# Performance work log

Hardware: AMD Instinct MI355X
Metric: run time of the kernel (lower is better)

Reference implementation:

```python
import jax, jax.numpy as jnp
import numpy as np


def setup_inputs() -> dict:
    key = jax.random.key(0)
    ks = jax.random.split(key, 6)
    B, d, S = 256, 512, 196  # batch, hidden dim, spatial locations (14x14)
    return {
        "memory_state": jax.random.normal(ks[0], (B, d), dtype=jnp.float32),
        "ctrl_state": jax.random.normal(ks[1], (B, d), dtype=jnp.float32),
        "kb_proj": jax.random.normal(ks[2], (B, d, S), dtype=jnp.float32),
        "W_concat": jax.random.normal(ks[3], (d, d), dtype=jnp.float32) * (1.0 / np.sqrt(d)),
        "b_concat": jax.random.normal(ks[4], (d,), dtype=jnp.float32) * 0.01,
        "w_attn": jax.random.normal(ks[5], (d,), dtype=jnp.float32) * (1.0 / np.sqrt(d)),
    }


def reference(memory_state, ctrl_state, kb_proj, W_concat, b_concat, w_attn):
    # I_elements: [B, S, d] -- elementwise gating of knowledge base by memory
    I_t = memory_state[:, :, None] * kb_proj           # [B, d, S]
    I_t = jnp.transpose(I_t, (0, 2, 1))                # [B, S, d]
    # concat_layer (torch Linear: x @ W^T + b) + residual with kb_proj
    concat = jnp.einsum('bsd,ed->bse', I_t, W_concat) + b_concat
    concat = concat + jnp.transpose(kb_proj, (0, 2, 1))  # [B, S, d]
    # attention logits: (concat * ctrl) @ w_attn -> [B, S]
    rai = jnp.einsum('bsd,d->bs', concat * ctrl_state[:, None, :], w_attn)
    rvi = jax.nn.softmax(rai, axis=1)                  # [B, S]
    # attention-weighted sum over spatial locations -> [B, d]
    read_vector = jnp.einsum('bs,bds->bd', rvi, kb_proj)
    return read_vector
```

## Files before the change

### kernel.cpp

```cpp
#include <hip/hip_runtime.h>
#include <math.h>

#define B 256
#define D 512
#define S 196
#define SQ 49
#define NCH 8

__global__ __launch_bounds__(256) void k_gemm(const float* __restrict__ ctrl,
                                              const float* __restrict__ w_attn,
                                              const float* __restrict__ W,
                                              float* __restrict__ gpart) {
    __shared__ float u_s[64][8];
    const int ce = blockIdx.x >> 5;
    const int b0 = (blockIdx.x & 31) * 8;
    const int t = threadIdx.x;
#pragma unroll
    for (int k = t; k < 512; k += 256) {
        const int j = k & 7, el = k >> 3;
        const int e = ce * 64 + el;
        u_s[el][j] = ctrl[(b0 + j) * D + e] * w_attn[e];
    }
    __syncthreads();
    float a0[8], a1[8];
#pragma unroll
    for (int j = 0; j < 8; ++j) { a0[j] = 0.f; a1[j] = 0.f; }
    for (int e0 = 0; e0 < 64; e0 += 4) {
        float w0[4], w1[4];
#pragma unroll
        for (int i = 0; i < 4; ++i) {
            const int e = ce * 64 + e0 + i;
            w0[i] = W[e * D + t];
            w1[i] = W[e * D + t + 256];
        }
#pragma unroll
        for (int i = 0; i < 4; ++i) {
            const float4 ua = *(const float4*)&u_s[e0 + i][0];
            const float4 ub = *(const float4*)&u_s[e0 + i][4];
            a0[0] += ua.x * w0[i]; a0[1] += ua.y * w0[i];
            a0[2] += ua.z * w0[i]; a0[3] += ua.w * w0[i];
            a0[4] += ub.x * w0[i]; a0[5] += ub.y * w0[i];
            a0[6] += ub.z * w0[i]; a0[7] += ub.w * w0[i];
            a1[0] += ua.x * w1[i]; a1[1] += ua.y * w1[i];
            a1[2] += ua.z * w1[i]; a1[3] += ua.w * w1[i];
            a1[4] += ub.x * w1[i]; a1[5] += ub.y * w1[i];
            a1[6] += ub.z * w1[i]; a1[7] += ub.w * w1[i];
        }
    }
#pragma unroll
    for (int j = 0; j < 8; ++j) {
        gpart[((size_t)(b0 + j) * NCH + ce) * D + t]       = a0[j];
        gpart[((size_t)(b0 + j) * NCH + ce) * D + t + 256] = a1[j];
    }
}

__global__ __launch_bounds__(256) void k_logits(const float* __restrict__ kb,
                                                const float* __restrict__ gpart,
                                                const float* __restrict__ mem,
                                                const float* __restrict__ ctrl,
                                                const float* __restrict__ w_attn,
                                                float* __restrict__ rai_part) {
    __shared__ float p_s[64];
    __shared__ float part[4][S];
    const int bid = blockIdx.x;
    const int b = bid >> 3, c = bid & 7;
    const int t = threadIdx.x;
    const int w = t >> 6, l = t & 63;
    if (t < 64) {
        const int d = c * 64 + t;
        float s = 0.f;
#pragma unroll
        for (int ce = 0; ce < NCH; ++ce)
            s += gpart[((size_t)b * NCH + ce) * D + d];
        p_s[t] = mem[b * D + d] * s + ctrl[b * D + d] * w_attn[d];
    }
    __syncthreads();
    const float* base = kb + (size_t)b * D * S + (size_t)c * 64 * S;
    if (l < SQ) {
        float4 acc0 = {0.f, 0.f, 0.f, 0.f}, acc1 = {0.f, 0.f, 0.f, 0.f};
        for (int i = 0; i < 8; ++i) {
            const int r0 = w * 16 + i, r1 = w * 16 + 8 + i;
            const float4 v0 = *(const float4*)(base + (size_t)r0 * S + 4 * l);
            const float4 v1 = *(const float4*)(base + (size_t)r1 * S + 4 * l);
            const float pv0 = p_s[r0], pv1 = p_s[r1];
            acc0.x += pv0 * v0.x; acc0.y += pv0 * v0.y;
            acc0.z += pv0 * v0.z; acc0.w += pv0 * v0.w;
            acc1.x += pv1 * v1.x; acc1.y += pv1 * v1.y;
            acc1.z += pv1 * v1.z; acc1.w += pv1 * v1.w;
        }
        part[w][4 * l + 0] = acc0.x + acc1.x;
        part[w][4 * l + 1] = acc0.y + acc1.y;
        part[w][4 * l + 2] = acc0.z + acc1.z;
        part[w][4 * l + 3] = acc0.w + acc1.w;
    }
    __syncthreads();
    if (t < S)
        rai_part[(size_t)bid * S + t] = (part[0][t] + part[1][t]) + (part[2][t] + part[3][t]);
}

__global__ __launch_bounds__(256) void k_wsum(const float* __restrict__ kb,
                                              const float* __restrict__ rai_part,
                                              float* __restrict__ out) {
    __shared__ float rvi_s[S];
    __shared__ float redm[4], reds[4];
    const int bid = blockIdx.x;
    const int b = bid >> 3, c = bid & 7;
    const int t = threadIdx.x;
    const int w = t >> 6, l = t & 63;
    float rai = -INFINITY;
    if (t < S) {
        float v = 0.f;
#pragma unroll
        for (int k = 0; k < NCH; ++k)
            v += rai_part[((size_t)b * NCH + k) * S + t];
        rai = v;
    }
    float m = rai;
#pragma unroll
    for (int o = 1; o < 64; o <<= 1) m = fmaxf(m, __shfl_xor(m, o, 64));
    if (l == 0) redm[w] = m;
    __syncthreads();
    m = fmaxf(fmaxf(redm[0], redm[1]), fmaxf(redm[2], redm[3]));
    float ex = (t < S) ? __expf(rai - m) : 0.f;
    float sm = ex;
#pragma unroll
    for (int o = 1; o < 64; o <<= 1) sm += __shfl_xor(sm, o, 64);
    if (l == 0) reds[w] = sm;
    __syncthreads();
    const float li = (reds[0] + reds[1]) + (reds[2] + reds[3]);
    if (t < S) rvi_s[t] = ex / li;
    __syncthreads();

    float4 rv = {0.f, 0.f, 0.f, 0.f};
    if (l < SQ) rv = *(const float4*)&rvi_s[4 * l];
    const float* base = kb + (size_t)b * D * S + (size_t)c * 64 * S;
#pragma unroll
    for (int i = 0; i < 8; ++i) {
        const int r0 = w * 16 + i, r1 = w * 16 + 8 + i;
        float a0 = 0.f, a1 = 0.f;
        if (l < SQ) {
            const float4 v0 = *(const float4*)(base + (size_t)r0 * S + 4 * l);
            const float4 v1 = *(const float4*)(base + (size_t)r1 * S + 4 * l);
            a0 = rv.x * v0.x + rv.y * v0.y + rv.z * v0.z + rv.w * v0.w;
            a1 = rv.x * v1.x + rv.y * v1.y + rv.z * v1.z + rv.w * v1.w;
        }
#pragma unroll
        for (int o = 1; o < 64; o <<= 1) {
            a0 += __shfl_xor(a0, o, 64);
            a1 += __shfl_xor(a1, o, 64);
        }
        if (l == 0) {
            out[(size_t)b * D + c * 64 + r0] = a0;
            out[(size_t)b * D + c * 64 + r1] = a1;
        }
    }
}

extern "C" void kernel_launch(void* const* d_in, const int* in_sizes, int n_in,
                              void* d_out, int out_size, void* d_ws, size_t ws_size,
                              hipStream_t stream) {
    const float* mem  = (const float*)d_in[0];
    const float* ctrl = (const float*)d_in[1];
    const float* kb   = (const float*)d_in[2];
    const float* W    = (const float*)d_in[3];
    const float* wat  = (const float*)d_in[5];
    float* out = (float*)d_out;

    float* gpart    = (float*)d_ws;
    float* rai_part = gpart + (size_t)B * NCH * D;

    k_gemm  <<<256,     256, 0, stream>>>(ctrl, wat, W, gpart);
    k_logits<<<B * NCH, 256, 0, stream>>>(kb, gpart, mem, ctrl, wat, rai_part);
    k_wsum  <<<B * NCH, 256, 0, stream>>>(kb, rai_part, out);
}
```

Baseline: 191.4 us.

## Fuse W-projection GEMM into logits kernel and use LDS reduction in weighted sum

Drops the separate GEMM kernel. Each logits block now computes its own 64-column slice of (ctrl*w_attn)·W directly from W, so the gpart buffer and one launch go away. The cost is redundant W reads: each (b,c) block reads a 512x64 slice of W, largely from L2. In the weighted-sum kernel, the per-row 64-lane shuffle reductions are replaced by writing partial dot products to shared memory followed by a segmented row reduction, and launch bounds are raised to request 8 blocks per CU.

```diff
diff --git a/kernel.cpp b/kernel.cpp
--- a/kernel.cpp
+++ b/kernel.cpp
@@ -7,74 +7,47 @@
 #define SQ 49
 #define NCH 8
 
-__global__ __launch_bounds__(256) void k_gemm(const float* __restrict__ ctrl,
-                                              const float* __restrict__ w_attn,
-                                              const float* __restrict__ W,
-                                              float* __restrict__ gpart) {
-    __shared__ float u_s[64][8];
-    const int ce = blockIdx.x >> 5;
-    const int b0 = (blockIdx.x & 31) * 8;
-    const int t = threadIdx.x;
-#pragma unroll
-    for (int k = t; k < 512; k += 256) {
-        const int j = k & 7, el = k >> 3;
-        const int e = ce * 64 + el;
-        u_s[el][j] = ctrl[(b0 + j) * D + e] * w_attn[e];
-    }
-    __syncthreads();
-    float a0[8], a1[8];
-#pragma unroll
-    for (int j = 0; j < 8; ++j) { a0[j] = 0.f; a1[j] = 0.f; }
-    for (int e0 = 0; e0 < 64; e0 += 4) {
-        float w0[4], w1[4];
-#pragma unroll
-        for (int i = 0; i < 4; ++i) {
-            const int e = ce * 64 + e0 + i;
-            w0[i] = W[e * D + t];
-            w1[i] = W[e * D + t + 256];
-        }
-#pragma unroll
-        for (int i = 0; i < 4; ++i) {
-            const float4 ua = *(const float4*)&u_s[e0 + i][0];
-            const float4 ub = *(const float4*)&u_s[e0 + i][4];
-            a0[0] += ua.x * w0[i]; a0[1] += ua.y * w0[i];
-            a0[2] += ua.z * w0[i]; a0[3] += ua.w * w0[i];
-            a0[4] += ub.x * w0[i]; a0[5] += ub.y * w0[i];
-            a0[6] += ub.z * w0[i]; a0[7] += ub.w * w0[i];
-            a1[0] += ua.x * w1[i]; a1[1] += ua.y * w1[i];
-            a1[2] += ua.z * w1[i]; a1[3] += ua.w * w1[i];
-            a1[4] += ub.x * w1[i]; a1[5] += ub.y * w1[i];
-            a1[6] += ub.z * w1[i]; a1[7] += ub.w * w1[i];
-        }
-    }
-#pragma unroll
-    for (int j = 0; j < 8; ++j) {
-        gpart[((size_t)(b0 + j) * NCH + ce) * D + t]       = a0[j];
-        gpart[((size_t)(b0 + j) * NCH + ce) * D + t + 256] = a1[j];
-    }
-}
-
-__global__ __launch_bounds__(256) void k_logits(const float* __restrict__ kb,
-                                                const float* __restrict__ gpart,
-                                                const float* __restrict__ mem,
-                                                const float* __restrict__ ctrl,
-                                                const float* __restrict__ w_attn,
-                                                float* __restrict__ rai_part) {
+__global__ __launch_bounds__(256, 8) void k_fused_logits(
+    const float* __restrict__ kb, const float* __restrict__ mem,
+    const float* __restrict__ ctrl, const float* __restrict__ w_attn,
+    const float* __restrict__ W, float* __restrict__ rai_part) {
+    __shared__ float u_s[D];
+    __shared__ float gred[16][64];
     __shared__ float p_s[64];
     __shared__ float part[4][S];
     const int bid = blockIdx.x;
     const int b = bid >> 3, c = bid & 7;
     const int t = threadIdx.x;
     const int w = t >> 6, l = t & 63;
-    if (t < 64) {
-        const int d = c * 64 + t;
-        float s = 0.f;
-#pragma unroll
-        for (int ce = 0; ce < NCH; ++ce)
-            s += gpart[((size_t)b * NCH + ce) * D + d];
-        p_s[t] = mem[b * D + d] * s + ctrl[b * D + d] * w_attn[d];
+
+    u_s[t]       = ctrl[(size_t)b * D + t]       * w_attn[t];
+    u_s[t + 256] = ctrl[(size_t)b * D + t + 256] * w_attn[t + 256];
+    __syncthreads();
+
+    {
+        const int q = t & 15, eg = t >> 4;
+        float4 g4 = {0.f, 0.f, 0.f, 0.f};
+        const float* wbase = W + (size_t)c * 64 + 4 * q;
+#pragma unroll 4
+        for (int k = 0; k < 32; ++k) {
+            const int e = k * 16 + eg;
+            const float4 w4 = *(const float4*)(wbase + (size_t)e * D);
+            const float uv = u_s[e];
+            g4.x += uv * w4.x; g4.y += uv * w4.y;
+            g4.z += uv * w4.z; g4.w += uv * w4.w;
+        }
+        *(float4*)&gred[eg][4 * q] = g4;
     }
     __syncthreads();
+    if (t < 64) {
+        float g = 0.f;
+#pragma unroll
+        for (int eg = 0; eg < 16; ++eg) g += gred[eg][t];
+        const int d = c * 64 + t;
+        p_s[t] = mem[(size_t)b * D + d] * g + u_s[d];
+    }
+    __syncthreads();
+
     const float* base = kb + (size_t)b * D * S + (size_t)c * 64 * S;
     if (l < SQ) {
         float4 acc0 = {0.f, 0.f, 0.f, 0.f}, acc1 = {0.f, 0.f, 0.f, 0.f};
@@ -95,18 +68,22 @@
     }
     __syncthreads();
     if (t < S)
-        rai_part[(size_t)bid * S + t] = (part[0][t] + part[1][t]) + (part[2][t] + part[3][t]);
+        rai_part[(size_t)bid * S + t] =
+            (part[0][t] + part[1][t]) + (part[2][t] + part[3][t]);
 }
 
-__global__ __launch_bounds__(256) void k_wsum(const float* __restrict__ kb,
-                                              const float* __restrict__ rai_part,
-                                              float* __restrict__ out) {
+__global__ __launch_bounds__(256, 8) void k_wsum(
+    const float* __restrict__ kb, const float* __restrict__ rai_part,
+    float* __restrict__ out) {
     __shared__ float rvi_s[S];
     __shared__ float redm[4], reds[4];
+    __shared__ float plds[64 * SQ];
+    __shared__ float red2[4][64];
     const int bid = blockIdx.x;
     const int b = bid >> 3, c = bid & 7;
     const int t = threadIdx.x;
     const int w = t >> 6, l = t & 63;
+
     float rai = -INFINITY;
     if (t < S) {
         float v = 0.f;
@@ -134,26 +111,30 @@
     float4 rv = {0.f, 0.f, 0.f, 0.f};
     if (l < SQ) rv = *(const float4*)&rvi_s[4 * l];
     const float* base = kb + (size_t)b * D * S + (size_t)c * 64 * S;
-#pragma unroll
-    for (int i = 0; i < 8; ++i) {
-        const int r0 = w * 16 + i, r1 = w * 16 + 8 + i;
-        float a0 = 0.f, a1 = 0.f;
-        if (l < SQ) {
+    if (l < SQ) {
+#pragma unroll 2
+        for (int i = 0; i < 8; ++i) {
+            const int r0 = w * 16 + i, r1 = w * 16 + 8 + i;
             const float4 v0 = *(const float4*)(base + (size_t)r0 * S + 4 * l);
             const float4 v1 = *(const float4*)(base + (size_t)r1 * S + 4 * l);
-            a0 = rv.x * v0.x + rv.y * v0.y + rv.z * v0.z + rv.w * v0.w;
-            a1 = rv.x * v1.x + rv.y * v1.y + rv.z * v1.z + rv.w * v1.w;
-        }
-#pragma unroll
-        for (int o = 1; o < 64; o <<= 1) {
-            a0 += __shfl_xor(a0, o, 64);
-            a1 += __shfl_xor(a1, o, 64);
-        }
-        if (l == 0) {
-            out[(size_t)b * D + c * 64 + r0] = a0;
-            out[(size_t)b * D + c * 64 + r1] = a1;
+            plds[r0 * SQ + l] =
+                rv.x * v0.x + rv.y * v0.y + rv.z * v0.z + rv.w * v0.w;
+            plds[r1 * SQ + l] =
+                rv.x * v1.x + rv.y * v1.y + rv.z * v1.z + rv.w * v1.w;
         }
     }
+    __syncthreads();
+    {
+        const int row = t & 63, seg = t >> 6;
+        const int j0 = (seg * SQ) >> 2, j1 = ((seg + 1) * SQ) >> 2;
+        float a = 0.f;
+        for (int j = j0; j < j1; ++j) a += plds[row * SQ + j];
+        red2[seg][row] = a;
+    }
+    __syncthreads();
+    if (t < 64)
+        out[(size_t)b * D + c * 64 + t] =
+            (red2[0][t] + red2[1][t]) + (red2[2][t] + red2[3][t]);
 }
 
 extern "C" void kernel_launch(void* const* d_in, const int* in_sizes, int n_in,
@@ -166,10 +147,8 @@
     const float* wat  = (const float*)d_in[5];
     float* out = (float*)d_out;
 
-    float* gpart    = (float*)d_ws;
-    float* rai_part = gpart + (size_t)B * NCH * D;
+    float* rai_part = (float*)d_ws;
 
-    k_gemm  <<<256,     256, 0, stream>>>(ctrl, wat, W, gpart);
-    k_logits<<<B * NCH, 256, 0, stream>>>(kb, gpart, mem, ctrl, wat, rai_part);
-    k_wsum  <<<B * NCH, 256, 0, stream>>>(kb, rai_part, out);
+    k_fused_logits<<<B * NCH, 256, 0, stream>>>(kb, mem, ctrl, wat, W, rai_part);
+    k_wsum        <<<B * NCH, 256, 0, stream>>>(kb, rai_part, out);
 }
```

After: 192.0 us. About the same (+0.3%).
